# Kernel tuning notes

Measured on AMD Instinct MI355X. Metric: run time of the kernel, lower is better.

The kernel has to match this reference:

```python
import jax, jax.numpy as jnp
import numpy as np

B, T, F = 1024, 512, 32
H, E, L = 128, 16, 2
N_TICKERS = 5000


def _gru_layer(x_seq, W_ih, W_hh, b_ih, b_hh):
    # x_seq: [B, T, I]; W_ih: [3H, I]; W_hh: [3H, H]. PyTorch gate order: r, z, n.
    gx = jnp.einsum('bti,gi->btg', x_seq, W_ih) + b_ih  # [B, T, 3H]

    def step(h, gx_t):
        gh = h @ W_hh.T + b_hh                     # [B, 3H]
        r = jax.nn.sigmoid(gx_t[:, :H] + gh[:, :H])
        z = jax.nn.sigmoid(gx_t[:, H:2 * H] + gh[:, H:2 * H])
        n = jnp.tanh(gx_t[:, 2 * H:] + r * gh[:, 2 * H:])
        h_new = (1.0 - z) * n + z * h
        return h_new, h_new

    h0 = jnp.zeros((x_seq.shape[0], H), dtype=x_seq.dtype)
    _, hs = jax.lax.scan(step, h0, jnp.swapaxes(gx, 0, 1))  # hs: [T, B, H]
    return jnp.swapaxes(hs, 0, 1)                            # [B, T, H]


def setup_inputs() -> dict:
    key = jax.random.key(0)
    ks = jax.random.split(key, 16)
    s_in0 = 1.0 / np.sqrt(H)
    inp = {
        'x': jax.random.normal(ks[0], (B, T, F), dtype=jnp.float32),
        'ticker_ids': jax.random.randint(ks[1], (B,), 0, N_TICKERS),
        'embed': jax.random.normal(ks[2], (N_TICKERS, E), dtype=jnp.float32),
        # GRU layer 0 (input size F+E=48)
        'W_ih0': jax.random.uniform(ks[3], (3 * H, F + E), minval=-s_in0, maxval=s_in0),
        'W_hh0': jax.random.uniform(ks[4], (3 * H, H), minval=-s_in0, maxval=s_in0),
        'b_ih0': jax.random.uniform(ks[5], (3 * H,), minval=-s_in0, maxval=s_in0),
        'b_hh0': jax.random.uniform(ks[6], (3 * H,), minval=-s_in0, maxval=s_in0),
        # GRU layer 1 (input size H)
        'W_ih1': jax.random.uniform(ks[7], (3 * H, H), minval=-s_in0, maxval=s_in0),
        'W_hh1': jax.random.uniform(ks[8], (3 * H, H), minval=-s_in0, maxval=s_in0),
        'b_ih1': jax.random.uniform(ks[9], (3 * H,), minval=-s_in0, maxval=s_in0),
        'b_hh1': jax.random.uniform(ks[10], (3 * H,), minval=-s_in0, maxval=s_in0),
        # head: Linear(H,H) -> ReLU -> Linear(H,1)
        'head_w1': jax.random.uniform(ks[11], (H, H), minval=-s_in0, maxval=s_in0),
        'head_b1': jax.random.uniform(ks[12], (H,), minval=-s_in0, maxval=s_in0),
        'head_w2': jax.random.uniform(ks[13], (1, H), minval=-s_in0, maxval=s_in0),
        'head_b2': jax.random.uniform(ks[14], (1,), minval=-s_in0, maxval=s_in0),
    }
    return inp


def reference(x, ticker_ids, embed, W_ih0, W_hh0, b_ih0, b_hh0,
              W_ih1, W_hh1, b_ih1, b_hh1, head_w1, head_b1, head_w2, head_b2):
    emb = embed[ticker_ids]                                  # [B, E]
    emb_seq = jnp.broadcast_to(emb[:, None, :], (x.shape[0], x.shape[1], emb.shape[-1]))
    xcat = jnp.concatenate([x, emb_seq], axis=-1)            # [B, T, F+E]
    h = _gru_layer(xcat, W_ih0, W_hh0, b_ih0, b_hh0)         # [B, T, H]
    h = _gru_layer(h, W_ih1, W_hh1, b_ih1, b_hh1)            # [B, T, H]
    last = h[:, -1, :]                                       # [B, H]
    hid = jax.nn.relu(last @ head_w1.T + head_b1)            # dropout inactive at eval
    y = (hid @ head_w2.T + head_b2)[:, 0]                    # [B]
    return y
```

## Files before the change

### kernel.cpp

```cpp
#include <hip/hip_runtime.h>

constexpr int kB  = 1024;
constexpr int kT  = 512;
constexpr int kF  = 32;
constexpr int kE  = 16;
constexpr int kH  = 128;
constexpr int kMB = 16;
constexpr int kNMB = kB / kMB;
constexpr int kTc = 32;
constexpr int kNCh = kT / kTc;
constexpr int kTg = kTc / 2;
constexpr size_t kH0Str = (size_t)kB * kTc * kH;
constexpr size_t kSlots = (size_t)kNMB * kTc * 512;

typedef __attribute__((ext_vector_type(8))) _Float16 f16x8;
typedef __attribute__((ext_vector_type(4))) _Float16 f16x4;
typedef __attribute__((ext_vector_type(4))) float    f32x4;

#define MFMA16(a,b,c) __builtin_amdgcn_mfma_f32_16x16x32_f16(a,b,c,0,0,0)

__device__ __forceinline__ float sigm_hw(float x){
    float e = __builtin_amdgcn_exp2f(-1.442695041f * x);
    return __builtin_amdgcn_rcpf(1.0f + e);
}
__device__ __forceinline__ float tanh_hw(float x){
    float e = __builtin_amdgcn_exp2f(-2.885390082f * x);
    return fmaf(2.0f, __builtin_amdgcn_rcpf(1.0f + e), -1.0f);
}
__device__ __forceinline__ void splitF(float v, _Float16 &hi, _Float16 &lo){
    hi = (_Float16)v;
    lo = (_Float16)(v - (float)hi);
}
__device__ __forceinline__ f16x8 loadW8(const float* __restrict__ p){
    f16x8 r;
#pragma unroll
    for (int j=0;j<8;j++) r[j] = (_Float16)p[j];
    return r;
}
__device__ __forceinline__ unsigned short f2u(_Float16 h){ return __builtin_bit_cast(unsigned short, h); }
__device__ __forceinline__ _Float16 u2f(unsigned short u){ return __builtin_bit_cast(_Float16, u); }
__device__ __forceinline__ unsigned pack2(float a, float b){
    return (unsigned)f2u((_Float16)a) | ((unsigned)f2u((_Float16)b) << 16);
}

struct SRec {
    alignas(16) _Float16 hH[2][16][136];
    alignas(16) _Float16 hL[2][16][136];
    alignas(16) _Float16 xHp[2][16][40];
    alignas(16) _Float16 xLp[2][16][40];
    alignas(16) float hf[16][132];
    alignas(16) float hf2[16][132];
};
struct SGem {
    alignas(16) _Float16 aH[2][16][136];
    alignas(16) _Float16 aL[2][16][136];
};
union SU { SRec r; SGem g; };

__attribute__((amdgpu_waves_per_eu(2, 2)))
__global__ void __launch_bounds__(512) rnn_fused(
    const float* __restrict__ x, const int* __restrict__ tick,
    const float* __restrict__ embed,
    const float* __restrict__ Wih0, const float* __restrict__ Whh0,
    const float* __restrict__ bih0, const float* __restrict__ bhh0,
    const float* __restrict__ Wih1, const float* __restrict__ bih1,
    const float* __restrict__ Whh1, const float* __restrict__ bhh1,
    const float* __restrict__ hw1, const float* __restrict__ hb1,
    const float* __restrict__ hw2, const float* __restrict__ hb2,
    unsigned* __restrict__ h0seq, unsigned* __restrict__ gxA,
    unsigned* __restrict__ gxB, float* __restrict__ h1state,
    float* __restrict__ out, int c)
{
    __shared__ SU sm;
    const int tid = threadIdx.x;
    const int w = tid >> 6, l = tid & 63, lm = l & 15, lq = l >> 4;
    const int i = 16*w + lm;
    const int cls[3] = { i, 128 + i, 256 + i };

    if (blockIdx.x < 64) {
        if (c >= kNCh) return;
        SRec &S = sm.r;
        const int mb = blockIdx.x, b0 = mb * kMB;
        unsigned* h0w = h0seq + (size_t)(c & 1) * kH0Str;

        f16x8 wv[3][4], xw[3];
#pragma unroll
        for (int T=0; T<3; T++){
#pragma unroll
            for (int kt=0; kt<4; kt++)
                wv[T][kt] = loadW8(Whh0 + (size_t)cls[T]*kH + kt*32 + lq*8);
            xw[T] = loadW8(Wih0 + (size_t)cls[T]*48 + lq*8);
        }
        float rIni[4], zIni[4], nxIni[4], nhIni;
        {
            float br = bih0[cls[0]] + bhh0[cls[0]];
            float bz = bih0[cls[1]] + bhh0[cls[1]];
            float bn = bih0[cls[2]];
            nhIni = bhh0[cls[2]];
            const float* w0 = Wih0 + (size_t)cls[0]*48 + 32;
            const float* w1 = Wih0 + (size_t)cls[1]*48 + 32;
            const float* w2 = Wih0 + (size_t)cls[2]*48 + 32;
#pragma unroll
            for (int q=0; q<4; q++){
                const float* ep = embed + (size_t)tick[b0 + lq*4 + q] * kE;
                float s0=0.f, s1=0.f, s2=0.f;
#pragma unroll
                for (int e=0; e<kE; e++){
                    float ev = ep[e];
                    s0 = fmaf(ev, w0[e], s0);
                    s1 = fmaf(ev, w1[e], s1);
                    s2 = fmaf(ev, w2[e], s2);
                }
                rIni[q]=br+s0; zIni[q]=bz+s1; nxIni[q]=bn+s2;
            }
        }
        float hreg[4];
        if (c == 0){
#pragma unroll
            for (int q=0;q<4;q++){
                hreg[q]=0.f;
                S.hH[0][lq*4+q][i]=(_Float16)0.f;
                S.hL[0][lq*4+q][i]=(_Float16)0.f;
            }
        } else {
            const unsigned* h0p = h0seq + (size_t)((c-1) & 1) * kH0Str;
#pragma unroll
            for (int q=0;q<4;q++){
                unsigned u = h0p[((size_t)(mb*kTc + kTc-1)*16 + lq*4+q)*kH + i];
                _Float16 hh = u2f((unsigned short)(u>>16)), hl = u2f((unsigned short)u);
                hreg[q] = (float)hh + (float)hl;
                S.hH[0][lq*4+q][i]=hh; S.hL[0][lq*4+q][i]=hl;
            }
        }
        const int xm = tid >> 5, xk = tid & 31;
        const size_t xbase = (size_t)(b0+xm)*kT*kF + xk;
        {
            _Float16 a2,b2; splitF(x[xbase + (size_t)(c*kTc)*kF], a2, b2);
            S.xHp[0][xm][xk]=a2; S.xLp[0][xm][xk]=b2;
        }
        int t1 = c*kTc + 1; if (t1 > kT-1) t1 = kT-1;
        float xnext = x[xbase + (size_t)t1*kF];
        __syncthreads();

        int buf = 0;
        for (int tc=0; tc<kTc; tc++){
            const int nb = buf ^ 1;
            f16x8 aHf[4], aLf[4];
#pragma unroll
            for (int kt=0;kt<4;kt++){
                aHf[kt] = *(const f16x8*)&S.hH[buf][lm][kt*32 + lq*8];
                aLf[kt] = *(const f16x8*)&S.hL[buf][lm][kt*32 + lq*8];
            }
            f16x8 xvH = *(const f16x8*)&S.xHp[buf][lm][lq*8];
            f16x8 xvL = *(const f16x8*)&S.xLp[buf][lm][lq*8];
            f32x4 aR ={rIni[0],rIni[1],rIni[2],rIni[3]};
            f32x4 aZ ={zIni[0],zIni[1],zIni[2],zIni[3]};
            f32x4 aNX={nxIni[0],nxIni[1],nxIni[2],nxIni[3]};
            f32x4 aNH={nhIni,nhIni,nhIni,nhIni};
#pragma unroll
            for (int kt=0;kt<4;kt++){
                aR =MFMA16(aHf[kt],wv[0][kt],aR);  aR =MFMA16(aLf[kt],wv[0][kt],aR);
                aZ =MFMA16(aHf[kt],wv[1][kt],aZ);  aZ =MFMA16(aLf[kt],wv[1][kt],aZ);
                aNH=MFMA16(aHf[kt],wv[2][kt],aNH); aNH=MFMA16(aLf[kt],wv[2][kt],aNH);
            }
            aR =MFMA16(xvH,xw[0],aR);  aR =MFMA16(xvL,xw[0],aR);
            aZ =MFMA16(xvH,xw[1],aZ);  aZ =MFMA16(xvL,xw[1],aZ);
            aNX=MFMA16(xvH,xw[2],aNX); aNX=MFMA16(xvL,xw[2],aNX);
            unsigned pk[4];
#pragma unroll
            for (int q=0;q<4;q++){
                float r = sigm_hw(aR[q]);
                float z = sigm_hw(aZ[q]);
                float n = tanh_hw(fmaf(r, aNH[q], aNX[q]));
                float h = fmaf(z, hreg[q]-n, n);
                hreg[q] = h;
                _Float16 hh,hl; splitF(h,hh,hl);
                S.hH[nb][lq*4+q][i]=hh;
                S.hL[nb][lq*4+q][i]=hl;
                pk[q] = ((unsigned)f2u(hh)<<16) | f2u(hl);
            }
#pragma unroll
            for (int q=0;q<4;q++)
                h0w[((size_t)(mb*kTc + tc)*16 + lq*4+q)*kH + i] = pk[q];
            {
                _Float16 a2,b2; splitF(xnext,a2,b2);
                S.xHp[nb][xm][xk]=a2; S.xLp[nb][xm][xk]=b2;
                int tn = c*kTc + tc + 2; if (tn > kT-1) tn = kT-1;
                xnext = x[xbase + (size_t)tn*kF];
            }
            __syncthreads();
            buf = nb;
        }
    } else if (blockIdx.x < 192) {
        const int g = c - 1;
        if (g < 0 || g >= kNCh) return;
        SGem &S = sm.g;
        const int bid = blockIdx.x - 64;
        const int mb = bid >> 1, t0 = (bid & 1) * kTg;
        const unsigned* h0r = h0seq + (size_t)(g & 1) * kH0Str;
        unsigned* gA = gxA + (size_t)(g & 1) * kSlots * 4;
        unsigned* gB = gxB + (size_t)(g & 1) * kSlots * 2;

        f16x8 wv[3][4]; float bI[3];
#pragma unroll
        for (int T=0; T<3; T++){
#pragma unroll
            for (int kt=0; kt<4; kt++)
                wv[T][kt] = loadW8(Wih1 + (size_t)cls[T]*kH + kt*32 + lq*8);
            bI[T] = bih1[cls[T]];
        }
        const int sr = tid >> 5, sq = tid & 31;
        auto ld = [&](int t){
            return *(const uint4*)(h0r + ((size_t)(mb*kTc + t)*16 + sr)*kH + 4*sq);
        };
        auto stage = [&](int bf, uint4 u){
            f16x4 vh = { u2f((unsigned short)(u.x>>16)), u2f((unsigned short)(u.y>>16)),
                         u2f((unsigned short)(u.z>>16)), u2f((unsigned short)(u.w>>16)) };
            f16x4 vl = { u2f((unsigned short)u.x), u2f((unsigned short)u.y),
                         u2f((unsigned short)u.z), u2f((unsigned short)u.w) };
            *(f16x4*)&S.aH[bf][sr][4*sq] = vh;
            *(f16x4*)&S.aL[bf][sr][4*sq] = vl;
        };
        stage(0, ld(t0));
        uint4 nxt = ld(t0 + 1);
        __syncthreads();
        for (int tt=0; tt<kTg; tt++){
            const int t = t0 + tt, bf = tt & 1;
            f16x8 fH[4], fL[4];
#pragma unroll
            for (int kt=0;kt<4;kt++){
                fH[kt] = *(const f16x8*)&S.aH[bf][lm][kt*32 + lq*8];
                fL[kt] = *(const f16x8*)&S.aL[bf][lm][kt*32 + lq*8];
            }
            if (tt+1 < kTg) stage(bf^1, nxt);
            if (tt+2 < kTg) nxt = ld(t0 + tt + 2);
            f32x4 aR = {bI[0],bI[0],bI[0],bI[0]};
            f32x4 aZ = {bI[1],bI[1],bI[1],bI[1]};
            f32x4 aN = {bI[2],bI[2],bI[2],bI[2]};
#pragma unroll
            for (int kt=0;kt<4;kt++){
                aR=MFMA16(fH[kt],wv[0][kt],aR); aR=MFMA16(fL[kt],wv[0][kt],aR);
                aZ=MFMA16(fH[kt],wv[1][kt],aZ); aZ=MFMA16(fL[kt],wv[1][kt],aZ);
                aN=MFMA16(fH[kt],wv[2][kt],aN); aN=MFMA16(fL[kt],wv[2][kt],aN);
            }
            const size_t slot = ((size_t)mb*kTc + t)*512 + tid;
            *(uint4*)(gA + slot*4) = make_uint4(pack2(aR[0],aR[1]), pack2(aR[2],aR[3]),
                                                pack2(aZ[0],aZ[1]), pack2(aZ[2],aZ[3]));
            *(uint2*)(gB + slot*2) = make_uint2(pack2(aN[0],aN[1]), pack2(aN[2],aN[3]));
            __syncthreads();
        }
    } else {
        const int e0 = c - 2;
        if (e0 < 0 || e0 >= kNCh) return;
        SRec &S = sm.r;
        const int mb = blockIdx.x - 192, b0 = mb * kMB;
        const unsigned* gA = gxA + (size_t)(e0 & 1) * kSlots * 4;
        const unsigned* gB = gxB + (size_t)(e0 & 1) * kSlots * 2;

        f16x8 wv[3][4];
#pragma unroll
        for (int T=0; T<3; T++)
#pragma unroll
            for (int kt=0; kt<4; kt++)
                wv[T][kt] = loadW8(Whh1 + (size_t)cls[T]*kH + kt*32 + lq*8);
        const float br = bhh1[cls[0]], bz = bhh1[cls[1]], bn = bhh1[cls[2]];

        float hreg[4];
        if (e0 == 0){
#pragma unroll
            for (int q=0;q<4;q++){
                hreg[q]=0.f;
                S.hH[0][lq*4+q][i]=(_Float16)0.f;
                S.hL[0][lq*4+q][i]=(_Float16)0.f;
            }
        } else {
#pragma unroll
            for (int q=0;q<4;q++){
                float h = h1state[(size_t)(b0 + lq*4+q)*kH + i];
                hreg[q]=h;
                _Float16 hh,hl; splitF(h,hh,hl);
                S.hH[0][lq*4+q][i]=hh; S.hL[0][lq*4+q][i]=hl;
            }
        }
        const size_t base = (size_t)mb*kTc*512 + tid;
        uint4 g4c = *(const uint4*)(gA + base*4);
        uint2 g2c = *(const uint2*)(gB + base*2);
        uint4 g4n = *(const uint4*)(gA + (base + 512)*4);
        uint2 g2n = *(const uint2*)(gB + (base + 512)*2);
        __syncthreads();

        int buf = 0;
        for (int tc=0; tc<kTc; tc++){
            const int nb = buf ^ 1;
            f16x8 aHf[4], aLf[4];
#pragma unroll
            for (int kt=0;kt<4;kt++){
                aHf[kt] = *(const f16x8*)&S.hH[buf][lm][kt*32 + lq*8];
                aLf[kt] = *(const f16x8*)&S.hL[buf][lm][kt*32 + lq*8];
            }
            f32x4 aR={br,br,br,br}, aZ={bz,bz,bz,bz}, aNH={bn,bn,bn,bn};
#pragma unroll
            for (int kt=0;kt<4;kt++){
                aR =MFMA16(aHf[kt],wv[0][kt],aR);  aR =MFMA16(aLf[kt],wv[0][kt],aR);
                aZ =MFMA16(aHf[kt],wv[1][kt],aZ);  aZ =MFMA16(aLf[kt],wv[1][kt],aZ);
                aNH=MFMA16(aHf[kt],wv[2][kt],aNH); aNH=MFMA16(aLf[kt],wv[2][kt],aNH);
            }
            const float rx[4] = { (float)u2f((unsigned short)g4c.x), (float)u2f((unsigned short)(g4c.x>>16)),
                                  (float)u2f((unsigned short)g4c.y), (float)u2f((unsigned short)(g4c.y>>16)) };
            const float zx[4] = { (float)u2f((unsigned short)g4c.z), (float)u2f((unsigned short)(g4c.z>>16)),
                                  (float)u2f((unsigned short)g4c.w), (float)u2f((unsigned short)(g4c.w>>16)) };
            const float nx[4] = { (float)u2f((unsigned short)g2c.x), (float)u2f((unsigned short)(g2c.x>>16)),
                                  (float)u2f((unsigned short)g2c.y), (float)u2f((unsigned short)(g2c.y>>16)) };
#pragma unroll
            for (int q=0;q<4;q++){
                float r = sigm_hw(aR[q] + rx[q]);
                float z = sigm_hw(aZ[q] + zx[q]);
                float n = tanh_hw(fmaf(r, aNH[q], nx[q]));
                float h = fmaf(z, hreg[q]-n, n);
                hreg[q] = h;
                _Float16 hh,hl; splitF(h,hh,hl);
                S.hH[nb][lq*4+q][i]=hh;
                S.hL[nb][lq*4+q][i]=hl;
            }
            g4c = g4n; g2c = g2n;
            int tn = tc + 2; if (tn > kTc-1) tn = kTc-1;
            g4n = *(const uint4*)(gA + (base + (size_t)tn*512)*4);
            g2n = *(const uint2*)(gB + (base + (size_t)tn*512)*2);
            __syncthreads();
            buf = nb;
        }
#pragma unroll
        for (int q=0;q<4;q++)
            h1state[(size_t)(b0 + lq*4+q)*kH + i] = hreg[q];
        if (e0 == kNCh-1){
#pragma unroll
            for (int q=0;q<4;q++) S.hf[lq*4+q][i] = hreg[q];
            __syncthreads();
            const int hm = tid >> 5, i0 = (tid & 31) * 4;
#pragma unroll
            for (int e=0;e<4;e++){
                const float* wr = hw1 + (size_t)(i0+e)*kH;
                float s = hb1[i0+e];
                for (int k2=0;k2<kH;k2++) s = fmaf(wr[k2], S.hf[hm][k2], s);
                S.hf2[hm][i0+e] = fmaxf(s, 0.f);
            }
            __syncthreads();
            if (tid < kMB){
                float s = hb2[0];
                for (int k2=0;k2<kH;k2++) s = fmaf(S.hf2[tid][k2], hw2[k2], s);
                out[b0 + tid] = s;
            }
        }
    }
}

extern "C" void kernel_launch(void* const* d_in, const int* in_sizes, int n_in,
                              void* d_out, int out_size, void* d_ws, size_t ws_size,
                              hipStream_t stream)
{
    const float* x     = (const float*)d_in[0];
    const int*   tick  = (const int*)d_in[1];
    const float* embed = (const float*)d_in[2];
    const float* Wih0  = (const float*)d_in[3];
    const float* Whh0  = (const float*)d_in[4];
    const float* bih0  = (const float*)d_in[5];
    const float* bhh0  = (const float*)d_in[6];
    const float* Wih1  = (const float*)d_in[7];
    const float* Whh1  = (const float*)d_in[8];
    const float* bih1  = (const float*)d_in[9];
    const float* bhh1  = (const float*)d_in[10];
    const float* hw1   = (const float*)d_in[11];
    const float* hb1   = (const float*)d_in[12];
    const float* hw2   = (const float*)d_in[13];
    const float* hb2   = (const float*)d_in[14];
    float* out = (float*)d_out;

    unsigned* h0seq = (unsigned*)d_ws;
    unsigned* gxA   = h0seq + 2*kH0Str;
    unsigned* gxB   = gxA + 2*kSlots*4;
    float*  h1state = (float*)(gxB + 2*kSlots*2);

    for (int c = 0; c <= kNCh + 1; c++){
        rnn_fused<<<256, 512, 0, stream>>>(x, tick, embed,
            Wih0, Whh0, bih0, bhh0, Wih1, bih1, Whh1, bhh1,
            hw1, hb1, hw2, hb2, h0seq, gxA, gxB, h1state, out, c);
    }
}
```

Measured before the change: 1.226 ms.

## Fuse layer-1 input projection into layer-0 recurrence blocks, drop h0 sequence buffer

The layer-1 input GEMM (W_ih1·h0) now runs inside the layer-0 recurrent blocks, one step behind, reusing the h0 fragments already in LDS. This removes the separate GEMM block group, the full h0 sequence write/read through global memory, and one pipeline stage of launches (17 instead of 18, with 128 blocks). Only a final h0 carry state is stored. Barriers are replaced with an lgkmcnt-wait plus s_barrier. The cost is more MFMA work and more weight registers on the serial layer-0 critical path.

```diff
diff --git a/kernel.cpp b/kernel.cpp
--- a/kernel.cpp
+++ b/kernel.cpp
@@ -9,12 +9,9 @@
 constexpr int kNMB = kB / kMB;
 constexpr int kTc = 32;
 constexpr int kNCh = kT / kTc;
-constexpr int kTg = kTc / 2;
-constexpr size_t kH0Str = (size_t)kB * kTc * kH;
 constexpr size_t kSlots = (size_t)kNMB * kTc * 512;
 
 typedef __attribute__((ext_vector_type(8))) _Float16 f16x8;
-typedef __attribute__((ext_vector_type(4))) _Float16 f16x4;
 typedef __attribute__((ext_vector_type(4))) float    f32x4;
 
 #define MFMA16(a,b,c) __builtin_amdgcn_mfma_f32_16x16x32_f16(a,b,c,0,0,0)
@@ -41,6 +38,9 @@
 __device__ __forceinline__ _Float16 u2f(unsigned short u){ return __builtin_bit_cast(_Float16, u); }
 __device__ __forceinline__ unsigned pack2(float a, float b){
     return (unsigned)f2u((_Float16)a) | ((unsigned)f2u((_Float16)b) << 16);
+}
+__device__ __forceinline__ void bar_lds(){
+    asm volatile("s_waitcnt lgkmcnt(0)\n\ts_barrier" ::: "memory");
 }
 
 struct SRec {
@@ -51,11 +51,6 @@
     alignas(16) float hf[16][132];
     alignas(16) float hf2[16][132];
 };
-struct SGem {
-    alignas(16) _Float16 aH[2][16][136];
-    alignas(16) _Float16 aL[2][16][136];
-};
-union SU { SRec r; SGem g; };
 
 __attribute__((amdgpu_waves_per_eu(2, 2)))
 __global__ void __launch_bounds__(512) rnn_fused(
@@ -67,11 +62,11 @@
     const float* __restrict__ Whh1, const float* __restrict__ bhh1,
     const float* __restrict__ hw1, const float* __restrict__ hb1,
     const float* __restrict__ hw2, const float* __restrict__ hb2,
-    unsigned* __restrict__ h0seq, unsigned* __restrict__ gxA,
-    unsigned* __restrict__ gxB, float* __restrict__ h1state,
+    unsigned* __restrict__ gxA, unsigned* __restrict__ gxB,
+    float* __restrict__ h0carry, float* __restrict__ h1state,
     float* __restrict__ out, int c)
 {
-    __shared__ SU sm;
+    __shared__ SRec S;
     const int tid = threadIdx.x;
     const int w = tid >> 6, l = tid & 63, lm = l & 15, lq = l >> 4;
     const int i = 16*w + lm;
@@ -79,19 +74,22 @@
 
     if (blockIdx.x < 64) {
         if (c >= kNCh) return;
-        SRec &S = sm.r;
         const int mb = blockIdx.x, b0 = mb * kMB;
-        unsigned* h0w = h0seq + (size_t)(c & 1) * kH0Str;
-
-        f16x8 wv[3][4], xw[3];
+        unsigned* gA = gxA + (size_t)(c & 1) * kSlots * 4;
+        unsigned* gB = gxB + (size_t)(c & 1) * kSlots * 2;
+
+        f16x8 wv[3][4], xw[3], wg[3][4];
 #pragma unroll
         for (int T=0; T<3; T++){
 #pragma unroll
-            for (int kt=0; kt<4; kt++)
+            for (int kt=0; kt<4; kt++){
                 wv[T][kt] = loadW8(Whh0 + (size_t)cls[T]*kH + kt*32 + lq*8);
+                wg[T][kt] = loadW8(Wih1 + (size_t)cls[T]*kH + kt*32 + lq*8);
+            }
             xw[T] = loadW8(Wih0 + (size_t)cls[T]*48 + lq*8);
         }
         float rIni[4], zIni[4], nxIni[4], nhIni;
+        const float gIni0 = bih1[cls[0]], gIni1 = bih1[cls[1]], gIni2 = bih1[cls[2]];
         {
             float br = bih0[cls[0]] + bhh0[cls[0]];
             float bz = bih0[cls[1]] + bhh0[cls[1]];
@@ -115,22 +113,12 @@
             }
         }
         float hreg[4];
-        if (c == 0){
-#pragma unroll
-            for (int q=0;q<4;q++){
-                hreg[q]=0.f;
-                S.hH[0][lq*4+q][i]=(_Float16)0.f;
-                S.hL[0][lq*4+q][i]=(_Float16)0.f;
-            }
-        } else {
-            const unsigned* h0p = h0seq + (size_t)((c-1) & 1) * kH0Str;
-#pragma unroll
-            for (int q=0;q<4;q++){
-                unsigned u = h0p[((size_t)(mb*kTc + kTc-1)*16 + lq*4+q)*kH + i];
-                _Float16 hh = u2f((unsigned short)(u>>16)), hl = u2f((unsigned short)u);
-                hreg[q] = (float)hh + (float)hl;
-                S.hH[0][lq*4+q][i]=hh; S.hL[0][lq*4+q][i]=hl;
-            }
+#pragma unroll
+        for (int q=0;q<4;q++){
+            float h = (c == 0) ? 0.f : h0carry[(size_t)(b0 + lq*4+q)*kH + i];
+            hreg[q] = h;
+            _Float16 hh,hl; splitF(h,hh,hl);
+            S.hH[0][lq*4+q][i]=hh; S.hL[0][lq*4+q][i]=hl;
         }
         const int xm = tid >> 5, xk = tid & 31;
         const size_t xbase = (size_t)(b0+xm)*kT*kF + xk;
@@ -140,120 +128,76 @@
         }
         int t1 = c*kTc + 1; if (t1 > kT-1) t1 = kT-1;
         float xnext = x[xbase + (size_t)t1*kF];
-        __syncthreads();
+        bar_lds();
 
         int buf = 0;
-        for (int tc=0; tc<kTc; tc++){
-            const int nb = buf ^ 1;
+        for (int it=0; it<=kTc; it++){
             f16x8 aHf[4], aLf[4];
 #pragma unroll
             for (int kt=0;kt<4;kt++){
                 aHf[kt] = *(const f16x8*)&S.hH[buf][lm][kt*32 + lq*8];
                 aLf[kt] = *(const f16x8*)&S.hL[buf][lm][kt*32 + lq*8];
             }
-            f16x8 xvH = *(const f16x8*)&S.xHp[buf][lm][lq*8];
-            f16x8 xvL = *(const f16x8*)&S.xLp[buf][lm][lq*8];
-            f32x4 aR ={rIni[0],rIni[1],rIni[2],rIni[3]};
-            f32x4 aZ ={zIni[0],zIni[1],zIni[2],zIni[3]};
-            f32x4 aNX={nxIni[0],nxIni[1],nxIni[2],nxIni[3]};
-            f32x4 aNH={nhIni,nhIni,nhIni,nhIni};
-#pragma unroll
-            for (int kt=0;kt<4;kt++){
-                aR =MFMA16(aHf[kt],wv[0][kt],aR);  aR =MFMA16(aLf[kt],wv[0][kt],aR);
-                aZ =MFMA16(aHf[kt],wv[1][kt],aZ);  aZ =MFMA16(aLf[kt],wv[1][kt],aZ);
-                aNH=MFMA16(aHf[kt],wv[2][kt],aNH); aNH=MFMA16(aLf[kt],wv[2][kt],aNH);
-            }
-            aR =MFMA16(xvH,xw[0],aR);  aR =MFMA16(xvL,xw[0],aR);
-            aZ =MFMA16(xvH,xw[1],aZ);  aZ =MFMA16(xvL,xw[1],aZ);
-            aNX=MFMA16(xvH,xw[2],aNX); aNX=MFMA16(xvL,xw[2],aNX);
-            unsigned pk[4];
-#pragma unroll
-            for (int q=0;q<4;q++){
-                float r = sigm_hw(aR[q]);
-                float z = sigm_hw(aZ[q]);
-                float n = tanh_hw(fmaf(r, aNH[q], aNX[q]));
-                float h = fmaf(z, hreg[q]-n, n);
-                hreg[q] = h;
-                _Float16 hh,hl; splitF(h,hh,hl);
-                S.hH[nb][lq*4+q][i]=hh;
-                S.hL[nb][lq*4+q][i]=hl;
-                pk[q] = ((unsigned)f2u(hh)<<16) | f2u(hl);
-            }
-#pragma unroll
-            for (int q=0;q<4;q++)
-                h0w[((size_t)(mb*kTc + tc)*16 + lq*4+q)*kH + i] = pk[q];
-            {
-                _Float16 a2,b2; splitF(xnext,a2,b2);
-                S.xHp[nb][xm][xk]=a2; S.xLp[nb][xm][xk]=b2;
-                int tn = c*kTc + tc + 2; if (tn > kT-1) tn = kT-1;
-                xnext = x[xbase + (size_t)tn*kF];
-            }
-            __syncthreads();
-            buf = nb;
-        }
-    } else if (blockIdx.x < 192) {
-        const int g = c - 1;
-        if (g < 0 || g >= kNCh) return;
-        SGem &S = sm.g;
-        const int bid = blockIdx.x - 64;
-        const int mb = bid >> 1, t0 = (bid & 1) * kTg;
-        const unsigned* h0r = h0seq + (size_t)(g & 1) * kH0Str;
-        unsigned* gA = gxA + (size_t)(g & 1) * kSlots * 4;
-        unsigned* gB = gxB + (size_t)(g & 1) * kSlots * 2;
-
-        f16x8 wv[3][4]; float bI[3];
-#pragma unroll
-        for (int T=0; T<3; T++){
-#pragma unroll
-            for (int kt=0; kt<4; kt++)
-                wv[T][kt] = loadW8(Wih1 + (size_t)cls[T]*kH + kt*32 + lq*8);
-            bI[T] = bih1[cls[T]];
-        }
-        const int sr = tid >> 5, sq = tid & 31;
-        auto ld = [&](int t){
-            return *(const uint4*)(h0r + ((size_t)(mb*kTc + t)*16 + sr)*kH + 4*sq);
-        };
-        auto stage = [&](int bf, uint4 u){
-            f16x4 vh = { u2f((unsigned short)(u.x>>16)), u2f((unsigned short)(u.y>>16)),
-                         u2f((unsigned short)(u.z>>16)), u2f((unsigned short)(u.w>>16)) };
-            f16x4 vl = { u2f((unsigned short)u.x), u2f((unsigned short)u.y),
-                         u2f((unsigned short)u.z), u2f((unsigned short)u.w) };
-            *(f16x4*)&S.aH[bf][sr][4*sq] = vh;
-            *(f16x4*)&S.aL[bf][sr][4*sq] = vl;
-        };
-        stage(0, ld(t0));
-        uint4 nxt = ld(t0 + 1);
-        __syncthreads();
-        for (int tt=0; tt<kTg; tt++){
-            const int t = t0 + tt, bf = tt & 1;
-            f16x8 fH[4], fL[4];
-#pragma unroll
-            for (int kt=0;kt<4;kt++){
-                fH[kt] = *(const f16x8*)&S.aH[bf][lm][kt*32 + lq*8];
-                fL[kt] = *(const f16x8*)&S.aL[bf][lm][kt*32 + lq*8];
-            }
-            if (tt+1 < kTg) stage(bf^1, nxt);
-            if (tt+2 < kTg) nxt = ld(t0 + tt + 2);
-            f32x4 aR = {bI[0],bI[0],bI[0],bI[0]};
-            f32x4 aZ = {bI[1],bI[1],bI[1],bI[1]};
-            f32x4 aN = {bI[2],bI[2],bI[2],bI[2]};
-#pragma unroll
-            for (int kt=0;kt<4;kt++){
-                aR=MFMA16(fH[kt],wv[0][kt],aR); aR=MFMA16(fL[kt],wv[0][kt],aR);
-                aZ=MFMA16(fH[kt],wv[1][kt],aZ); aZ=MFMA16(fL[kt],wv[1][kt],aZ);
-                aN=MFMA16(fH[kt],wv[2][kt],aN); aN=MFMA16(fL[kt],wv[2][kt],aN);
-            }
-            const size_t slot = ((size_t)mb*kTc + t)*512 + tid;
-            *(uint4*)(gA + slot*4) = make_uint4(pack2(aR[0],aR[1]), pack2(aR[2],aR[3]),
-                                                pack2(aZ[0],aZ[1]), pack2(aZ[2],aZ[3]));
-            *(uint2*)(gB + slot*2) = make_uint2(pack2(aN[0],aN[1]), pack2(aN[2],aN[3]));
-            __syncthreads();
-        }
+            if (it >= 1){
+                f32x4 gR={gIni0,gIni0,gIni0,gIni0};
+                f32x4 gZ={gIni1,gIni1,gIni1,gIni1};
+                f32x4 gN={gIni2,gIni2,gIni2,gIni2};
+#pragma unroll
+                for (int kt=0;kt<4;kt++){
+                    gR=MFMA16(aHf[kt],wg[0][kt],gR); gR=MFMA16(aLf[kt],wg[0][kt],gR);
+                    gZ=MFMA16(aHf[kt],wg[1][kt],gZ); gZ=MFMA16(aLf[kt],wg[1][kt],gZ);
+                    gN=MFMA16(aHf[kt],wg[2][kt],gN); gN=MFMA16(aLf[kt],wg[2][kt],gN);
+                }
+                const size_t slot = ((size_t)mb*kTc + (it-1))*512 + tid;
+                *(uint4*)(gA + slot*4) = make_uint4(pack2(gR[0],gR[1]), pack2(gR[2],gR[3]),
+                                                    pack2(gZ[0],gZ[1]), pack2(gZ[2],gZ[3]));
+                *(uint2*)(gB + slot*2) = make_uint2(pack2(gN[0],gN[1]), pack2(gN[2],gN[3]));
+            }
+            if (it < kTc){
+                const int nb = buf ^ 1;
+                f16x8 xvH = *(const f16x8*)&S.xHp[buf][lm][lq*8];
+                f16x8 xvL = *(const f16x8*)&S.xLp[buf][lm][lq*8];
+                f32x4 aR ={rIni[0],rIni[1],rIni[2],rIni[3]};
+                f32x4 aZ ={zIni[0],zIni[1],zIni[2],zIni[3]};
+                f32x4 aNX={nxIni[0],nxIni[1],nxIni[2],nxIni[3]};
+                f32x4 aNH={nhIni,nhIni,nhIni,nhIni};
+#pragma unroll
+                for (int kt=0;kt<4;kt++){
+                    aR =MFMA16(aHf[kt],wv[0][kt],aR);  aR =MFMA16(aLf[kt],wv[0][kt],aR);
+                    aZ =MFMA16(aHf[kt],wv[1][kt],aZ);  aZ =MFMA16(aLf[kt],wv[1][kt],aZ);
+                    aNH=MFMA16(aHf[kt],wv[2][kt],aNH); aNH=MFMA16(aLf[kt],wv[2][kt],aNH);
+                }
+                aR =MFMA16(xvH,xw[0],aR);  aR =MFMA16(xvL,xw[0],aR);
+                aZ =MFMA16(xvH,xw[1],aZ);  aZ =MFMA16(xvL,xw[1],aZ);
+                aNX=MFMA16(xvH,xw[2],aNX); aNX=MFMA16(xvL,xw[2],aNX);
+#pragma unroll
+                for (int q=0;q<4;q++){
+                    float r = sigm_hw(aR[q]);
+                    float z = sigm_hw(aZ[q]);
+                    float n = tanh_hw(fmaf(r, aNH[q], aNX[q]));
+                    float h = fmaf(z, hreg[q]-n, n);
+                    hreg[q] = h;
+                    _Float16 hh,hl; splitF(h,hh,hl);
+                    S.hH[nb][lq*4+q][i]=hh;
+                    S.hL[nb][lq*4+q][i]=hl;
+                }
+                {
+                    _Float16 a2,b2; splitF(xnext,a2,b2);
+                    S.xHp[nb][xm][xk]=a2; S.xLp[nb][xm][xk]=b2;
+                    int tn = c*kTc + it + 2; if (tn > kT-1) tn = kT-1;
+                    xnext = x[xbase + (size_t)tn*kF];
+                }
+                bar_lds();
+                buf = nb;
+            }
+        }
+#pragma unroll
+        for (int q=0;q<4;q++)
+            h0carry[(size_t)(b0 + lq*4+q)*kH + i] = hreg[q];
     } else {
-        const int e0 = c - 2;
+        const int e0 = c - 1;
         if (e0 < 0 || e0 >= kNCh) return;
-        SRec &S = sm.r;
-        const int mb = blockIdx.x - 192, b0 = mb * kMB;
+        const int mb = blockIdx.x - 64, b0 = mb * kMB;
         const unsigned* gA = gxA + (size_t)(e0 & 1) * kSlots * 4;
         const unsigned* gB = gxB + (size_t)(e0 & 1) * kSlots * 2;
 
@@ -266,28 +210,19 @@
         const float br = bhh1[cls[0]], bz = bhh1[cls[1]], bn = bhh1[cls[2]];
 
         float hreg[4];
-        if (e0 == 0){
-#pragma unroll
-            for (int q=0;q<4;q++){
-                hreg[q]=0.f;
-                S.hH[0][lq*4+q][i]=(_Float16)0.f;
-                S.hL[0][lq*4+q][i]=(_Float16)0.f;
-            }
-        } else {
-#pragma unroll
-            for (int q=0;q<4;q++){
-                float h = h1state[(size_t)(b0 + lq*4+q)*kH + i];
-                hreg[q]=h;
-                _Float16 hh,hl; splitF(h,hh,hl);
-                S.hH[0][lq*4+q][i]=hh; S.hL[0][lq*4+q][i]=hl;
-            }
+#pragma unroll
+        for (int q=0;q<4;q++){
+            float h = (e0 == 0) ? 0.f : h1state[(size_t)(b0 + lq*4+q)*kH + i];
+            hreg[q]=h;
+            _Float16 hh,hl; splitF(h,hh,hl);
+            S.hH[0][lq*4+q][i]=hh; S.hL[0][lq*4+q][i]=hl;
         }
         const size_t base = (size_t)mb*kTc*512 + tid;
         uint4 g4c = *(const uint4*)(gA + base*4);
         uint2 g2c = *(const uint2*)(gB + base*2);
         uint4 g4n = *(const uint4*)(gA + (base + 512)*4);
         uint2 g2n = *(const uint2*)(gB + (base + 512)*2);
-        __syncthreads();
+        bar_lds();
 
         int buf = 0;
         for (int tc=0; tc<kTc; tc++){
@@ -326,7 +261,7 @@
             int tn = tc + 2; if (tn > kTc-1) tn = kTc-1;
             g4n = *(const uint4*)(gA + (base + (size_t)tn*512)*4);
             g2n = *(const uint2*)(gB + (base + (size_t)tn*512)*2);
-            __syncthreads();
+            bar_lds();
             buf = nb;
         }
 #pragma unroll
@@ -375,14 +310,14 @@
     const float* hb2   = (const float*)d_in[14];
     float* out = (float*)d_out;
 
-    unsigned* h0seq = (unsigned*)d_ws;
-    unsigned* gxA   = h0seq + 2*kH0Str;
+    unsigned* gxA   = (unsigned*)d_ws;
     unsigned* gxB   = gxA + 2*kSlots*4;
-    float*  h1state = (float*)(gxB + 2*kSlots*2);
-
-    for (int c = 0; c <= kNCh + 1; c++){
-        rnn_fused<<<256, 512, 0, stream>>>(x, tick, embed,
+    float*  h0carry = (float*)(gxB + 2*kSlots*2);
+    float*  h1state = h0carry + (size_t)kB*kH;
+
+    for (int c = 0; c <= kNCh; c++){
+        rnn_fused<<<128, 512, 0, stream>>>(x, tick, embed,
             Wih0, Whh0, bih0, bhh0, Wih1, bih1, Whh1, bhh1,
-            hw1, hb1, hw2, hb2, h0seq, gxA, gxB, h1state, out, c);
+            hw1, hb1, hw2, hb2, gxA, gxB, h0carry, h1state, out, c);
     }
 }
```

Result: slower. 1.660 ms (+35.4%).
